# Kernel tuning notes

Hardware: AMD Instinct MI355X
Metric: run time of the kernel (lower is better)

The kernel has to match this reference:

```python
import jax, jax.numpy as jnp
import numpy as np

PI = float(np.pi)


def _layernorm(x, g, b, eps=1e-5):
    mu = jnp.mean(x, axis=-1, keepdims=True)
    var = jnp.var(x, axis=-1, keepdims=True)
    return (x - mu) * jax.lax.rsqrt(var + eps) * g + b


def setup_inputs() -> dict:
    key = jax.random.key(0)
    B, L, D, P = 4, 2048, 256, 32
    ks = jax.random.split(key, 16)

    def lin_w(k, fi, fo):
        return (jax.random.normal(k, (fi, fo), dtype=jnp.float32) / np.sqrt(fi)).astype(jnp.float32)

    inp = {
        'x': jax.random.normal(ks[0], (B, L, D), dtype=jnp.float32),
        'pos_phases': jax.random.normal(ks[1], (L, P), dtype=jnp.float32) * PI,
        'w_mem1v': lin_w(ks[2], D, P), 'b_mem1v': jnp.zeros((P,), jnp.float32),
        'w_mem1o': lin_w(ks[3], P, D), 'b_mem1o': jnp.zeros((D,), jnp.float32),
        'w_off': lin_w(ks[4], D + P, P), 'b_off': jnp.zeros((P,), jnp.float32),
        'w_key': lin_w(ks[5], D, P), 'b_key': jnp.zeros((P,), jnp.float32),
        'w_val': lin_w(ks[6], D, D), 'b_val': jnp.zeros((D,), jnp.float32),
        'w_sk1': lin_w(ks[7], 2 * D, D), 'b_sk1': jnp.zeros((D,), jnp.float32),
        'w_sk2': lin_w(ks[8], D, P), 'b_sk2': jnp.zeros((P,), jnp.float32),
        'w_gate': lin_w(ks[9], D, 1), 'b_gate': jnp.zeros((1,), jnp.float32),
        'ln_g': jnp.ones((D,), jnp.float32), 'ln_b': jnp.zeros((D,), jnp.float32),
        'w_out': lin_w(ks[10], D, D), 'b_out': jnp.zeros((D,), jnp.float32),
    }
    return inp


def reference(x, pos_phases, w_mem1v, b_mem1v, w_mem1o, b_mem1o, w_off, b_off,
              w_key, b_key, w_val, b_val, w_sk1, b_sk1, w_sk2, b_sk2,
              w_gate, b_gate, ln_g, ln_b, w_out, b_out):
    B, L, D = x.shape
    P = pos_phases.shape[-1]

    pos_cos = jnp.cos(pos_phases)  # [L,P]
    pos_sin = jnp.sin(pos_phases)

    # Memory 1: flat [B,L,P] phasor cumulative memory
    v1 = x @ w_mem1v + b_mem1v                       # [B,L,P]
    mem1_cos = jnp.cumsum(pos_cos[None] * v1, axis=1)
    mem1_sin = jnp.cumsum(pos_sin[None] * v1, axis=1)

    offset_input = jnp.concatenate([x, jnp.broadcast_to(pos_phases[None], (B, L, P))], axis=-1)
    offset = jnp.tanh(offset_input @ w_off + b_off) * PI
    oc, os = jnp.cos(offset), jnp.sin(offset)
    query_cos = pos_cos[None] * oc - pos_sin[None] * os
    query_sin = pos_sin[None] * oc + pos_cos[None] * os
    pos_ret = (mem1_cos * query_cos + mem1_sin * query_sin) / np.sqrt(P)
    pos_out = pos_ret @ w_mem1o + b_mem1o            # [B,L,D]

    # Memory 2: full [B,L,P,D] phasor KV cumulative memory
    key_phases = jnp.tanh(x @ w_key + b_key) * PI    # [B,L,P]
    key_cos, key_sin = jnp.cos(key_phases), jnp.sin(key_phases)
    values = x @ w_val + b_val                       # [B,L,D]
    store_gate = jax.nn.sigmoid(x @ w_gate + b_gate) # [B,L,1]

    positions = jnp.arange(1, L + 1, dtype=x.dtype)[None, :, None]
    context_avg = jnp.cumsum(x, axis=1) / positions
    h = jax.nn.gelu(jnp.concatenate([x, context_avg], axis=-1) @ w_sk1 + b_sk1, approximate=False)
    storage_phases = jnp.tanh(h @ w_sk2 + b_sk2) * PI  # [B,L,P]

    gated_v = values * store_gate                    # [B,L,D]
    kv_mem_cos = jnp.cumsum(jnp.cos(storage_phases)[..., None] * gated_v[:, :, None, :], axis=1)  # [B,L,P,D]
    kv_mem_sin = jnp.cumsum(jnp.sin(storage_phases)[..., None] * gated_v[:, :, None, :], axis=1)

    gate_cumsum = jnp.clip(jnp.cumsum(store_gate, axis=1), 1.0, None)  # [B,L,1]
    kv_retrieved = jnp.einsum('blpd,blp->bld', kv_mem_cos, key_cos) + \
                   jnp.einsum('blpd,blp->bld', kv_mem_sin, key_sin)
    kv_retrieved = kv_retrieved / (jnp.sqrt(gate_cumsum) * np.sqrt(P))

    combined = pos_out + kv_retrieved
    return x + _layernorm(combined, ln_g, ln_b) @ w_out + b_out
```

## Files before the change

kernel.cpp:

```cpp
#include <hip/hip_runtime.h>
#include <hip/hip_bf16.h>

constexpr int B_ = 4;
constexpr int L_ = 2048;
constexpr int D_ = 256;
constexpr int P_ = 32;
constexpr int CL = 32;
constexpr int NC = L_ / CL;

#define PI_F 3.14159265358979323846f
#define INV_SQRT_P 0.17677669529663687f

typedef __attribute__((ext_vector_type(8))) short short8_t;
typedef __attribute__((ext_vector_type(4))) float floatx4;

static __device__ inline short f2bf(float f) {
  unsigned int u;
  __builtin_memcpy(&u, &f, 4);
  unsigned int r = (u + 0x7fffu + ((u >> 16) & 1u)) >> 16;
  return (short)r;
}
static __device__ inline float bf2f(short s) {
  unsigned int u = ((unsigned int)(unsigned short)s) << 16;
  float f;
  __builtin_memcpy(&f, &u, 4);
  return f;
}

__global__ void wprep(const float* __restrict__ x, const float* __restrict__ pos,
                      const float* __restrict__ w_val, const float* __restrict__ w_mem1v,
                      const float* __restrict__ w_off, const float* __restrict__ b_off,
                      const float* __restrict__ w_key, const float* __restrict__ w_gate,
                      const float* __restrict__ w_sk1, const float* __restrict__ w_out,
                      const float* __restrict__ w_sk2, const float* __restrict__ w_mem1o,
                      short* __restrict__ WA, short* __restrict__ W1,
                      short* __restrict__ WO, short* __restrict__ W2T,
                      short* __restrict__ W1OT,
                      short* __restrict__ xbf, float* __restrict__ poff,
                      float* __restrict__ ctxsum) {
  int blk = blockIdx.x, tid = threadIdx.x;
  if (blk < 384) {
    int idx = blk * 256 + tid;
    int n = idx >> 8, k = idx & 255;
    float v;
    if (n < 256) v = w_val[k * 256 + n];
    else if (n < 288) v = w_mem1v[k * 32 + (n - 256)];
    else if (n < 320) v = w_off[k * 32 + (n - 288)];
    else if (n < 352) v = w_key[k * 32 + (n - 320)];
    else if (n == 352) v = w_gate[k];
    else v = 0.f;
    WA[idx] = f2bf(v);
  } else if (blk < 896) {
    int idx = (blk - 384) * 256 + tid;
    int n = idx >> 9, k = idx & 511;
    W1[idx] = f2bf(w_sk1[k * 256 + n]);
  } else if (blk < 1152) {
    int idx = (blk - 896) * 256 + tid;
    int n = idx >> 8, k = idx & 255;
    WO[idx] = f2bf(w_out[k * 256 + n]);
  } else if (blk < 1184) {
    int idx = (blk - 1152) * 256 + tid;
    int p = idx >> 8, k = idx & 255;
    W2T[idx] = f2bf(w_sk2[k * 32 + p]);
  } else if (blk < 1216) {
    int idx = (blk - 1184) * 256 + tid;
    int d = idx >> 5, p = idx & 31;
    W1OT[idx] = f2bf(w_mem1o[p * 256 + d]);
  } else if (blk < 3264) {
    int idx = ((blk - 1216) * 256 + tid) * 4;
    float4 v = *(const float4*)&x[idx];
    short4 o;
    o.x = f2bf(v.x); o.y = f2bf(v.y); o.z = f2bf(v.z); o.w = f2bf(v.w);
    *(short4*)&xbf[idx] = o;
  } else if (blk < 3520) {
    int idx = (blk - 3264) * 256 + tid;
    int l = idx >> 5, p = idx & 31;
    float a = b_off[p];
    for (int j = 0; j < 32; ++j) a += pos[l * 32 + j] * w_off[(256 + j) * 32 + p];
    poff[idx] = a;
  } else {
    int c2 = blk - 3520;
    int b = c2 >> 6, ch = c2 & 63;
    int xb = (b * L_ + ch * 32) * 256 + tid;
    float s = 0.f;
#pragma unroll 8
    for (int i = 0; i < 32; ++i) s += x[xb + i * 256];
    ctxsum[c2 * 256 + tid] = s;
  }
}

template <int KTILES, int NBLK, int MODE>
__global__ __launch_bounds__(256) void gemm_k(const short* __restrict__ A0,
                                              const short* __restrict__ A1,
                                              const short* __restrict__ W,
                                              const float* __restrict__ bias,
                                              const float* __restrict__ xres,
                                              float* __restrict__ outf,
                                              short* __restrict__ outb) {
  __shared__ short As[64][136];
  __shared__ short Bs[64][136];
  int tid = threadIdx.x;
  int mg = blockIdx.x / NBLK, ng = blockIdx.x % NBLK;
  int tok0 = mg * 64, n0 = ng * 64;
  int lane = tid & 63, w = tid >> 6;
  int mw = (w & 1) * 32, nw = (w >> 1) * 32;
  floatx4 acc[2][2] = {{{0.f, 0.f, 0.f, 0.f}, {0.f, 0.f, 0.f, 0.f}},
                       {{0.f, 0.f, 0.f, 0.f}, {0.f, 0.f, 0.f, 0.f}}};
  int r2 = tid >> 4, c8 = tid & 15;
  int ml = lane & 15, kq = (lane >> 4) * 8;
  const int K = KTILES * 128;

  for (int kt = 0; kt < KTILES; ++kt) {
    const short* Asrc;
    int cb;
    if (KTILES == 4) {
      Asrc = (kt < 2) ? A0 : A1;
      cb = (kt & 1) * 128;
    } else {
      Asrc = A0;
      cb = kt * 128;
    }
#pragma unroll
    for (int pass = 0; pass < 4; ++pass) {
      int row = pass * 16 + r2;
      *(short8_t*)&As[row][c8 * 8] =
          *(const short8_t*)&Asrc[(tok0 + row) * 256 + cb + c8 * 8];
      *(short8_t*)&Bs[row][c8 * 8] =
          *(const short8_t*)&W[(n0 + row) * K + kt * 128 + c8 * 8];
    }
    __syncthreads();
#pragma unroll
    for (int s = 0; s < 4; ++s) {
      short8_t a0 = *(short8_t*)&As[mw + ml][s * 32 + kq];
      short8_t a1 = *(short8_t*)&As[mw + 16 + ml][s * 32 + kq];
      short8_t b0 = *(short8_t*)&Bs[nw + ml][s * 32 + kq];
      short8_t b1 = *(short8_t*)&Bs[nw + 16 + ml][s * 32 + kq];
      acc[0][0] = __builtin_amdgcn_mfma_f32_16x16x32_bf16(a0, b0, acc[0][0], 0, 0, 0);
      acc[0][1] = __builtin_amdgcn_mfma_f32_16x16x32_bf16(a0, b1, acc[0][1], 0, 0, 0);
      acc[1][0] = __builtin_amdgcn_mfma_f32_16x16x32_bf16(a1, b0, acc[1][0], 0, 0, 0);
      acc[1][1] = __builtin_amdgcn_mfma_f32_16x16x32_bf16(a1, b1, acc[1][1], 0, 0, 0);
    }
    __syncthreads();
  }
  int col = lane & 15, rq = (lane >> 4) * 4;
#pragma unroll
  for (int nt = 0; nt < 2; ++nt) {
    int n = n0 + nw + nt * 16 + col;
    float bv = (MODE == 0) ? 0.f : bias[n];
#pragma unroll
    for (int mt = 0; mt < 2; ++mt) {
#pragma unroll
      for (int rg = 0; rg < 4; ++rg) {
        int tok = tok0 + mw + mt * 16 + rq + rg;
        float v = acc[mt][nt][rg] + bv;
        if (MODE == 0) {
          outb[tok * 384 + n] = f2bf(v);
        } else if (MODE == 1) {
          float g = 0.5f * v * (1.f + erff(v * 0.70710678118654752f));
          outb[tok * 256 + n] = f2bf(g);
        } else {
          outf[tok * 256 + n] = xres[tok * 256 + n] + v;
        }
      }
    }
  }
}

__global__ __launch_bounds__(384) void gemmA3(const short* __restrict__ xbf,
                                              const short* __restrict__ WA,
                                              const float* __restrict__ pos,
                                              const float* __restrict__ poff,
                                              const float* __restrict__ b_mem1v,
                                              const float* __restrict__ b_key,
                                              const float* __restrict__ b_gate,
                                              const float* __restrict__ b_val,
                                              float* __restrict__ m1cT,
                                              float* __restrict__ m1sT,
                                              float* __restrict__ qc,
                                              float* __restrict__ qs,
                                              short* __restrict__ K2bf,
                                              short* __restrict__ gvT,
                                              float* __restrict__ sg) {
  __shared__ float YL[32][132];
  __shared__ float gsh[32];
  int tid = threadIdx.x;
  int lane = tid & 63, w = tid >> 6;
  int ml = lane & 15, quad = lane >> 4, kq = quad * 8;
  int bc = blockIdx.x;
  int tok0 = bc * 32;
  floatx4 acc[2][4] = {};
  const short* A0p = &xbf[(tok0 + ml) * 256 + kq];
  const short* A1p = &xbf[(tok0 + 16 + ml) * 256 + kq];
  const short* Bp = &WA[(w * 64 + ml) * 256 + kq];
#pragma unroll
  for (int ks = 0; ks < 8; ++ks) {
    short8_t a0 = *(const short8_t*)(A0p + ks * 32);
    short8_t a1 = *(const short8_t*)(A1p + ks * 32);
#pragma unroll
    for (int nt = 0; nt < 4; ++nt) {
      short8_t b = *(const short8_t*)(Bp + nt * 16 * 256 + ks * 32);
      acc[0][nt] = __builtin_amdgcn_mfma_f32_16x16x32_bf16(a0, b, acc[0][nt], 0, 0, 0);
      acc[1][nt] = __builtin_amdgcn_mfma_f32_16x16x32_bf16(a1, b, acc[1][nt], 0, 0, 0);
    }
  }
  if (w >= 4) {
#pragma unroll
    for (int mt = 0; mt < 2; ++mt)
#pragma unroll
      for (int nt = 0; nt < 4; ++nt) {
        int col = (w - 4) * 64 + nt * 16 + ml;
#pragma unroll
        for (int r = 0; r < 4; ++r)
          YL[mt * 16 + quad * 4 + r][col] = acc[mt][nt][r];
      }
  }
  __syncthreads();
  if (tid < 256) {
#pragma unroll
    for (int it = 0; it < 4; ++it) {
      int idx = it * 256 + tid;
      int t = idx >> 5, p = idx & 31;
      int tok = tok0 + t, l = tok & (L_ - 1);
      int b = tok >> 11;
      float v1 = YL[t][p] + b_mem1v[p];
      float ph = pos[l * 32 + p];
      float pc = cosf(ph), ps = sinf(ph);
      int idxT = (b * 32 + p) * L_ + l;
      m1cT[idxT] = pc * v1;
      m1sT[idxT] = ps * v1;
      float off = tanhf(YL[t][32 + p] + poff[l * 32 + p]) * PI_F;
      float oc = cosf(off), os = sinf(off);
      int gidx = tok * 32 + p;
      qc[gidx] = pc * oc - ps * os;
      qs[gidx] = ps * oc + pc * os;
      float kp = tanhf(YL[t][64 + p] + b_key[p]) * PI_F;
      K2bf[tok * 64 + p] = f2bf(cosf(kp));
      K2bf[tok * 64 + 32 + p] = f2bf(sinf(kp));
      if (p == 0) {
        float g = 1.f / (1.f + expf(-(YL[t][96] + b_gate[0])));
        sg[tok] = g;
        gsh[t] = g;
      }
    }
  }
  __syncthreads();
  if (w < 4) {
#pragma unroll
    for (int nt = 0; nt < 4; ++nt) {
      int d = w * 64 + nt * 16 + ml;
      float bv = b_val[d];
#pragma unroll
      for (int mt = 0; mt < 2; ++mt) {
        int t0 = mt * 16 + quad * 4;
        short4 o;
        o.x = f2bf((acc[mt][nt][0] + bv) * gsh[t0 + 0]);
        o.y = f2bf((acc[mt][nt][1] + bv) * gsh[t0 + 1]);
        o.z = f2bf((acc[mt][nt][2] + bv) * gsh[t0 + 2]);
        o.w = f2bf((acc[mt][nt][3] + bv) * gsh[t0 + 3]);
        *(short4*)&gvT[(bc * 256 + d) * 32 + t0] = o;
      }
    }
  }
}

__global__ void scan_all(float* __restrict__ m1cT, float* __restrict__ m1sT,
                         float* __restrict__ sg, const float* __restrict__ x,
                         const float* __restrict__ ctxsum, short* __restrict__ ctxbf) {
  int blk = blockIdx.x;
  int tid = threadIdx.x;
  if (blk >= 260) {
    int c2 = blk - 260;
    int b = c2 >> 6, ch = c2 & 63;
    float run = 0.f;
    int sb = b * 64 * 256 + tid;
    for (int c = 0; c < ch; ++c) run += ctxsum[sb + c * 256];
    int xb = (b * L_ + ch * 32) * 256 + tid;
#pragma unroll 8
    for (int i = 0; i < 32; ++i) {
      run += x[xb + i * 256];
      int l = ch * 32 + i;
      ctxbf[xb + i * 256] = f2bf(run / (float)(l + 1));
    }
    return;
  }
  int lane = tid & 63, wid = tid >> 6;
  __shared__ float wsum[4];
  float carry = 0.f;
  float* arr;
  int base;
  if (blk < 256) {
    arr = (blk < 128) ? m1cT : m1sT;
    base = (blk & 127) * L_;
  } else {
    arr = sg;
    base = (blk - 256) * L_;
  }
  float v[8];
#pragma unroll
  for (int i = 0; i < 8; ++i) v[i] = arr[base + i * 256 + tid];
#pragma unroll
  for (int i = 0; i < 8; ++i) {
    float vv = v[i];
#pragma unroll
    for (int off = 1; off < 64; off <<= 1) {
      float n = __shfl_up(vv, off, 64);
      if (lane >= off) vv += n;
    }
    if (lane == 63) wsum[wid] = vv;
    __syncthreads();
    float add = carry;
    for (int w = 0; w < wid; ++w) add += wsum[w];
    arr[base + i * 256 + tid] = vv + add;
    carry += wsum[0] + wsum[1] + wsum[2] + wsum[3];
    __syncthreads();
  }
}

__global__ __launch_bounds__(256) void kernelCD(const short* __restrict__ hs,
                                                const short* __restrict__ W2T,
                                                const float* __restrict__ b_sk2,
                                                const short* __restrict__ gvT,
                                                short* __restrict__ SPbf,
                                                short* __restrict__ UT) {
  __shared__ __align__(16) short SPL[64][40];
  int tid = threadIdx.x;
  int bc = blockIdx.x;
  int tok0 = bc * 32;
  int lane = tid & 63, w = tid >> 6;
  int ml = lane & 15, quad = lane >> 4, kq = quad * 8;
  int th = w & 1, ph = w >> 1;
  floatx4 pacc = {};
#pragma unroll
  for (int s = 0; s < 8; ++s) {
    short8_t a = *(const short8_t*)&hs[(tok0 + th * 16 + ml) * 256 + s * 32 + kq];
    short8_t b0 = *(const short8_t*)&W2T[(ph * 16 + ml) * 256 + s * 32 + kq];
    pacc = __builtin_amdgcn_mfma_f32_16x16x32_bf16(a, b0, pacc, 0, 0, 0);
  }
  {
    int p = ph * 16 + ml;
    float bs = b_sk2[p];
#pragma unroll
    for (int r = 0; r < 4; ++r) {
      int tl = th * 16 + quad * 4 + r;
      int tok = tok0 + tl;
      float sp = tanhf(pacc[r] + bs) * PI_F;
      short c = f2bf(cosf(sp)), s = f2bf(sinf(sp));
      SPL[p][tl] = c;
      SPL[32 + p][tl] = s;
      SPbf[tok * 64 + p] = c;
      SPbf[tok * 64 + 32 + p] = s;
    }
  }
  __syncthreads();
  short8_t a[4];
#pragma unroll
  for (int mt = 0; mt < 4; ++mt) a[mt] = *(short8_t*)&SPL[mt * 16 + ml][kq];
  floatx4 acc[4][4] = {};
#pragma unroll
  for (int nt = 0; nt < 4; ++nt) {
    short8_t b = *(const short8_t*)&gvT[(bc * 256 + w * 64 + nt * 16 + ml) * 32 + kq];
#pragma unroll
    for (int mt = 0; mt < 4; ++mt)
      acc[mt][nt] = __builtin_amdgcn_mfma_f32_16x16x32_bf16(a[mt], b, acc[mt][nt], 0, 0, 0);
  }
#pragma unroll
  for (int mt = 0; mt < 4; ++mt)
#pragma unroll
    for (int nt = 0; nt < 4; ++nt)
#pragma unroll
      for (int r = 0; r < 4; ++r) {
        int q = mt * 16 + quad * 4 + r;
        int d = w * 64 + nt * 16 + ml;
        UT[(bc * 256 + d) * 64 + q] = f2bf(acc[mt][nt][r]);
      }
}

__global__ void kernelE(short* __restrict__ UT) {
  int tid = blockIdx.x * 256 + threadIdx.x;
  int q = tid & 63;
  int d = (tid >> 6) & 255;
  int b = tid >> 14;
  int base = ((b * NC) * 256 + d) * 64 + q;
  const int cs = 256 * 64;
  short v[64];
#pragma unroll
  for (int c = 0; c < 64; ++c) v[c] = UT[base + c * cs];
  float run = 0.f;
#pragma unroll
  for (int c = 0; c < 64; ++c) {
    UT[base + c * cs] = f2bf(run);
    run += bf2f(v[c]);
  }
}

__global__ __launch_bounds__(512) void kernelFG(const short* __restrict__ UT,
                                                const short* __restrict__ SPbf,
                                                const short* __restrict__ K2bf,
                                                const short* __restrict__ gvT,
                                                const float* __restrict__ sgc,
                                                const float* __restrict__ m1cT,
                                                const float* __restrict__ m1sT,
                                                const float* __restrict__ qc,
                                                const float* __restrict__ qs,
                                                const short* __restrict__ W1OT,
                                                const float* __restrict__ b_mem1o,
                                                const float* __restrict__ ln_g,
                                                const float* __restrict__ ln_b,
                                                short* __restrict__ cbn) {
  __shared__ __align__(16) short SL[32][40];
  __shared__ __align__(16) short PR[32][40];
  __shared__ float CMB[32][260];
  __shared__ float scl[32], mu_s[32], rs_s[32];
  int tid = threadIdx.x;
  int bc = blockIdx.x;
  int lbase = bc * CL;
  int bb = bc >> 6, lloc = (bc & 63) * 32;
  if (tid < 32) scl[tid] = rsqrtf(fmaxf(sgc[lbase + tid], 1.f)) * INV_SQRT_P;
#pragma unroll
  for (int it = 0; it < 2; ++it) {
    int i = it * 512 + tid;
    int p = i >> 5, t = i & 31;
    int gT = (bb * 32 + p) * L_ + lloc + t;
    int g = (lbase + t) * 32 + p;
    PR[t][p] = f2bf((m1cT[gT] * qc[g] + m1sT[gT] * qs[g]) * INV_SQRT_P);
  }
  int lane = tid & 63, w = tid >> 6;
  int ml = lane & 15, quad = lane >> 4, kq = quad * 8;
  int d0 = w * 32;
  floatx4 acc[2][2] = {};
  short8_t ka0 = *(const short8_t*)&K2bf[(lbase + ml) * 64 + kq];
  short8_t ka1 = *(const short8_t*)&K2bf[(lbase + 16 + ml) * 64 + kq];
  short8_t kb0 = *(const short8_t*)&K2bf[(lbase + ml) * 64 + 32 + kq];
  short8_t kb1 = *(const short8_t*)&K2bf[(lbase + 16 + ml) * 64 + 32 + kq];
#pragma unroll
  for (int nt = 0; nt < 2; ++nt) {
    short8_t b = *(const short8_t*)&UT[(bc * 256 + d0 + nt * 16 + ml) * 64 + kq];
    acc[0][nt] = __builtin_amdgcn_mfma_f32_16x16x32_bf16(ka0, b, acc[0][nt], 0, 0, 0);
    acc[1][nt] = __builtin_amdgcn_mfma_f32_16x16x32_bf16(ka1, b, acc[1][nt], 0, 0, 0);
  }
  if (w == 0) {
    floatx4 sacc[2][2] = {};
#pragma unroll
    for (int ks2 = 0; ks2 < 2; ++ks2) {
      short8_t a0 = (ks2 == 0) ? ka0 : kb0;
      short8_t a1 = (ks2 == 0) ? ka1 : kb1;
      short8_t b0 = *(const short8_t*)&SPbf[(lbase + ml) * 64 + ks2 * 32 + kq];
      short8_t b1 = *(const short8_t*)&SPbf[(lbase + 16 + ml) * 64 + ks2 * 32 + kq];
      sacc[0][0] = __builtin_amdgcn_mfma_f32_16x16x32_bf16(a0, b0, sacc[0][0], 0, 0, 0);
      sacc[0][1] = __builtin_amdgcn_mfma_f32_16x16x32_bf16(a0, b1, sacc[0][1], 0, 0, 0);
      sacc[1][0] = __builtin_amdgcn_mfma_f32_16x16x32_bf16(a1, b0, sacc[1][0], 0, 0, 0);
      sacc[1][1] = __builtin_amdgcn_mfma_f32_16x16x32_bf16(a1, b1, sacc[1][1], 0, 0, 0);
    }
#pragma unroll
    for (int mt = 0; mt < 2; ++mt)
#pragma unroll
      for (int nt = 0; nt < 2; ++nt)
#pragma unroll
        for (int r = 0; r < 4; ++r) {
          int trow = mt * 16 + quad * 4 + r;
          int scol = nt * 16 + ml;
          float v = (scol <= trow) ? sacc[mt][nt][r] : 0.f;
          SL[trow][scol] = f2bf(v);
        }
  }
  __syncthreads();
#pragma unroll
  for (int nt = 0; nt < 2; ++nt) {
    short8_t b = *(const short8_t*)&UT[(bc * 256 + d0 + nt * 16 + ml) * 64 + 32 + kq];
    acc[0][nt] = __builtin_amdgcn_mfma_f32_16x16x32_bf16(kb0, b, acc[0][nt], 0, 0, 0);
    acc[1][nt] = __builtin_amdgcn_mfma_f32_16x16x32_bf16(kb1, b, acc[1][nt], 0, 0, 0);
  }
  {
    short8_t a0 = *(short8_t*)&SL[ml][kq];
    short8_t a1 = *(short8_t*)&SL[16 + ml][kq];
#pragma unroll
    for (int nt = 0; nt < 2; ++nt) {
      short8_t b = *(const short8_t*)&gvT[(bc * 256 + d0 + nt * 16 + ml) * 32 + kq];
      acc[0][nt] = __builtin_amdgcn_mfma_f32_16x16x32_bf16(a0, b, acc[0][nt], 0, 0, 0);
      acc[1][nt] = __builtin_amdgcn_mfma_f32_16x16x32_bf16(a1, b, acc[1][nt], 0, 0, 0);
    }
  }
  floatx4 macc[2][2] = {};
  {
    short8_t a0 = *(short8_t*)&PR[ml][kq];
    short8_t a1 = *(short8_t*)&PR[16 + ml][kq];
#pragma unroll
    for (int nt = 0; nt < 2; ++nt) {
      short8_t b = *(const short8_t*)&W1OT[(d0 + nt * 16 + ml) * 32 + kq];
      macc[0][nt] = __builtin_amdgcn_mfma_f32_16x16x32_bf16(a0, b, macc[0][nt], 0, 0, 0);
      macc[1][nt] = __builtin_amdgcn_mfma_f32_16x16x32_bf16(a1, b, macc[1][nt], 0, 0, 0);
    }
  }
#pragma unroll
  for (int mt = 0; mt < 2; ++mt)
#pragma unroll
    for (int nt = 0; nt < 2; ++nt) {
      int d = d0 + nt * 16 + ml;
      float bm = b_mem1o[d];
#pragma unroll
      for (int r = 0; r < 4; ++r) {
        int t = mt * 16 + quad * 4 + r;
        CMB[t][d] = acc[mt][nt][r] * scl[t] + macc[mt][nt][r] + bm;
      }
    }
  __syncthreads();
  {
    int t = tid >> 4, g = tid & 15;
    float s = 0.f, s2 = 0.f;
#pragma unroll
    for (int j = 0; j < 16; ++j) {
      float v = CMB[t][g + j * 16];
      s += v;
      s2 += v * v;
    }
#pragma unroll
    for (int m = 1; m < 16; m <<= 1) {
      s += __shfl_xor(s, m, 64);
      s2 += __shfl_xor(s2, m, 64);
    }
    if (g == 0) {
      float mu = s / (float)D_;
      float var = s2 / (float)D_ - mu * mu;
      mu_s[t] = mu;
      rs_s[t] = rsqrtf(var + 1e-5f);
    }
  }
  __syncthreads();
  {
    int d = tid & 255, th = tid >> 8;
    float lg = ln_g[d], lb = ln_b[d];
#pragma unroll
    for (int i = 0; i < 16; ++i) {
      int t = th * 16 + i;
      cbn[(lbase + t) * 256 + d] = f2bf((CMB[t][d] - mu_s[t]) * rs_s[t] * lg + lb);
    }
  }
}

extern "C" void kernel_launch(void* const* d_in, const int* in_sizes, int n_in,
                              void* d_out, int out_size, void* d_ws, size_t ws_size,
                              hipStream_t stream) {
  const float* x = (const float*)d_in[0];
  const float* pos = (const float*)d_in[1];
  const float* w_mem1v = (const float*)d_in[2];
  const float* b_mem1v = (const float*)d_in[3];
  const float* w_mem1o = (const float*)d_in[4];
  const float* b_mem1o = (const float*)d_in[5];
  const float* w_off = (const float*)d_in[6];
  const float* b_off = (const float*)d_in[7];
  const float* w_key = (const float*)d_in[8];
  const float* b_key = (const float*)d_in[9];
  const float* w_val = (const float*)d_in[10];
  const float* b_val = (const float*)d_in[11];
  const float* w_sk1 = (const float*)d_in[12];
  const float* b_sk1 = (const float*)d_in[13];
  const float* w_sk2 = (const float*)d_in[14];
  const float* b_sk2 = (const float*)d_in[15];
  const float* w_gate = (const float*)d_in[16];
  const float* b_gate = (const float*)d_in[17];
  const float* ln_g = (const float*)d_in[18];
  const float* ln_b = (const float*)d_in[19];
  const float* w_out = (const float*)d_in[20];
  const float* b_out = (const float*)d_in[21];
  float* out = (float*)d_out;
  float* ws = (float*)d_ws;

  const int BLP = B_ * L_ * P_;
  const int BLD = B_ * L_ * D_;
  float* m1cT = ws;
  float* m1sT = m1cT + BLP;
  float* qc = m1sT + BLP;
  float* qs = qc + BLP;
  float* sg = qs + BLP;
  float* poff = sg + B_ * L_;
  float* ctxsum = poff + L_ * P_;
  short* UT = (short*)(ctxsum + B_ * 64 * 256);
  short* xbf = UT + (size_t)B_ * NC * 256 * 64;
  short* cbn = xbf;
  short* ctxbf = xbf + BLD;
  short* hs = ctxbf + BLD;
  short* gvT = hs + BLD;
  short* K2bf = gvT + BLD;
  short* SPbf = K2bf + B_ * L_ * 64;
  short* WA = SPbf + B_ * L_ * 64;
  short* W1 = WA + 384 * 256;
  short* WO = W1 + 256 * 512;
  short* W2T = WO + 256 * 256;
  short* W1OT = W2T + 32 * 256;

  wprep<<<3776, 256, 0, stream>>>(x, pos, w_val, w_mem1v, w_off, b_off, w_key, w_gate,
                                  w_sk1, w_out, w_sk2, w_mem1o, WA, W1, WO, W2T, W1OT,
                                  xbf, poff, ctxsum);
  gemmA3<<<256, 384, 0, stream>>>(xbf, WA, pos, poff, b_mem1v, b_key, b_gate, b_val,
                                  m1cT, m1sT, qc, qs, K2bf, gvT, sg);
  scan_all<<<516, 256, 0, stream>>>(m1cT, m1sT, sg, x, ctxsum, ctxbf);
  gemm_k<4, 4, 1><<<128 * 4, 256, 0, stream>>>(xbf, ctxbf, W1, b_sk1, nullptr, nullptr, hs);
  kernelCD<<<(B_ * L_) / 32, 256, 0, stream>>>(hs, W2T, b_sk2, gvT, SPbf, UT);
  kernelE<<<256, 256, 0, stream>>>(UT);
  kernelFG<<<B_ * NC, 512, 0, stream>>>(UT, SPbf, K2bf, gvT, sg, m1cT, m1sT, qc, qs,
                                        W1OT, b_mem1o, ln_g, ln_b, cbn);
  gemm_k<2, 4, 2><<<128 * 4, 256, 0, stream>>>(cbn, nullptr, WO, b_out, x, out, nullptr);
}
```

Baseline: 180.3 us.

## Halve tile sizes across GEMM and chunk kernels to double grid parallelism

The generic GEMM is replaced by a 32-token tile variant, launched on twice as many blocks. gemmA3 now processes 16 tokens per block, and kernelCD splits the D dimension across two blocks, with only one of them writing SPbf. UT stores are vectorised to short4, the ctxsum prefix loop is unrolled by eight, and occupancy hints are added to launch_bounds. The aim is to fill more of the MI355X's compute units on these small launches, at the cost of more redundant weight loads and lower MFMA reuse per block.

```diff
diff --git a/kernel.cpp b/kernel.cpp
--- a/kernel.cpp
+++ b/kernel.cpp
@@ -76,6 +76,7 @@
     int idx = (blk - 3264) * 256 + tid;
     int l = idx >> 5, p = idx & 31;
     float a = b_off[p];
+#pragma unroll 8
     for (int j = 0; j < 32; ++j) a += pos[l * 32 + j] * w_off[(256 + j) * 32 + p];
     poff[idx] = a;
   } else {
@@ -89,25 +90,24 @@
   }
 }
 
-template <int KTILES, int NBLK, int MODE>
-__global__ __launch_bounds__(256) void gemm_k(const short* __restrict__ A0,
-                                              const short* __restrict__ A1,
-                                              const short* __restrict__ W,
-                                              const float* __restrict__ bias,
-                                              const float* __restrict__ xres,
-                                              float* __restrict__ outf,
-                                              short* __restrict__ outb) {
-  __shared__ short As[64][136];
+template <int KTILES, int MODE>
+__global__ __launch_bounds__(256, 4) void gemm32(const short* __restrict__ A0,
+                                                 const short* __restrict__ A1,
+                                                 const short* __restrict__ W,
+                                                 const float* __restrict__ bias,
+                                                 const float* __restrict__ xres,
+                                                 float* __restrict__ outf,
+                                                 short* __restrict__ outb) {
+  __shared__ short As[32][136];
   __shared__ short Bs[64][136];
   int tid = threadIdx.x;
-  int mg = blockIdx.x / NBLK, ng = blockIdx.x % NBLK;
-  int tok0 = mg * 64, n0 = ng * 64;
+  int mg = blockIdx.x >> 2, ng = blockIdx.x & 3;
+  int tok0 = mg * 32, n0 = ng * 64;
   int lane = tid & 63, w = tid >> 6;
-  int mw = (w & 1) * 32, nw = (w >> 1) * 32;
-  floatx4 acc[2][2] = {{{0.f, 0.f, 0.f, 0.f}, {0.f, 0.f, 0.f, 0.f}},
-                       {{0.f, 0.f, 0.f, 0.f}, {0.f, 0.f, 0.f, 0.f}}};
+  int nw = w * 16;
+  floatx4 acc[2] = {{0.f, 0.f, 0.f, 0.f}, {0.f, 0.f, 0.f, 0.f}};
   int r2 = tid >> 4, c8 = tid & 15;
-  int ml = lane & 15, kq = (lane >> 4) * 8;
+  int ml = lane & 15, quad = lane >> 4, kq = quad * 8;
   const int K = KTILES * 128;
 
   for (int kt = 0; kt < KTILES; ++kt) {
@@ -121,103 +121,94 @@
       cb = kt * 128;
     }
 #pragma unroll
-    for (int pass = 0; pass < 4; ++pass) {
+    for (int pass = 0; pass < 2; ++pass) {
       int row = pass * 16 + r2;
       *(short8_t*)&As[row][c8 * 8] =
           *(const short8_t*)&Asrc[(tok0 + row) * 256 + cb + c8 * 8];
+    }
+#pragma unroll
+    for (int pass = 0; pass < 4; ++pass) {
+      int row = pass * 16 + r2;
       *(short8_t*)&Bs[row][c8 * 8] =
           *(const short8_t*)&W[(n0 + row) * K + kt * 128 + c8 * 8];
     }
     __syncthreads();
 #pragma unroll
     for (int s = 0; s < 4; ++s) {
-      short8_t a0 = *(short8_t*)&As[mw + ml][s * 32 + kq];
-      short8_t a1 = *(short8_t*)&As[mw + 16 + ml][s * 32 + kq];
+      short8_t a0 = *(short8_t*)&As[ml][s * 32 + kq];
+      short8_t a1 = *(short8_t*)&As[16 + ml][s * 32 + kq];
       short8_t b0 = *(short8_t*)&Bs[nw + ml][s * 32 + kq];
-      short8_t b1 = *(short8_t*)&Bs[nw + 16 + ml][s * 32 + kq];
-      acc[0][0] = __builtin_amdgcn_mfma_f32_16x16x32_bf16(a0, b0, acc[0][0], 0, 0, 0);
-      acc[0][1] = __builtin_amdgcn_mfma_f32_16x16x32_bf16(a0, b1, acc[0][1], 0, 0, 0);
-      acc[1][0] = __builtin_amdgcn_mfma_f32_16x16x32_bf16(a1, b0, acc[1][0], 0, 0, 0);
-      acc[1][1] = __builtin_amdgcn_mfma_f32_16x16x32_bf16(a1, b1, acc[1][1], 0, 0, 0);
+      acc[0] = __builtin_amdgcn_mfma_f32_16x16x32_bf16(a0, b0, acc[0], 0, 0, 0);
+      acc[1] = __builtin_amdgcn_mfma_f32_16x16x32_bf16(a1, b0, acc[1], 0, 0, 0);
     }
     __syncthreads();
   }
-  int col = lane & 15, rq = (lane >> 4) * 4;
-#pragma unroll
-  for (int nt = 0; nt < 2; ++nt) {
-    int n = n0 + nw + nt * 16 + col;
-    float bv = (MODE == 0) ? 0.f : bias[n];
-#pragma unroll
-    for (int mt = 0; mt < 2; ++mt) {
-#pragma unroll
-      for (int rg = 0; rg < 4; ++rg) {
-        int tok = tok0 + mw + mt * 16 + rq + rg;
-        float v = acc[mt][nt][rg] + bv;
-        if (MODE == 0) {
-          outb[tok * 384 + n] = f2bf(v);
-        } else if (MODE == 1) {
-          float g = 0.5f * v * (1.f + erff(v * 0.70710678118654752f));
-          outb[tok * 256 + n] = f2bf(g);
-        } else {
-          outf[tok * 256 + n] = xres[tok * 256 + n] + v;
-        }
+  int n = n0 + nw + ml;
+  float bv = bias ? bias[n] : 0.f;
+#pragma unroll
+  for (int mt = 0; mt < 2; ++mt) {
+#pragma unroll
+    for (int rg = 0; rg < 4; ++rg) {
+      int tok = tok0 + mt * 16 + quad * 4 + rg;
+      float v = acc[mt][rg] + bv;
+      if (MODE == 1) {
+        float g = 0.5f * v * (1.f + erff(v * 0.70710678118654752f));
+        outb[tok * 256 + n] = f2bf(g);
+      } else {
+        outf[tok * 256 + n] = xres[tok * 256 + n] + v;
       }
     }
   }
 }
 
-__global__ __launch_bounds__(384) void gemmA3(const short* __restrict__ xbf,
-                                              const short* __restrict__ WA,
-                                              const float* __restrict__ pos,
-                                              const float* __restrict__ poff,
-                                              const float* __restrict__ b_mem1v,
-                                              const float* __restrict__ b_key,
-                                              const float* __restrict__ b_gate,
-                                              const float* __restrict__ b_val,
-                                              float* __restrict__ m1cT,
-                                              float* __restrict__ m1sT,
-                                              float* __restrict__ qc,
-                                              float* __restrict__ qs,
-                                              short* __restrict__ K2bf,
-                                              short* __restrict__ gvT,
-                                              float* __restrict__ sg) {
-  __shared__ float YL[32][132];
-  __shared__ float gsh[32];
+__global__ __launch_bounds__(384, 3) void gemmA3(const short* __restrict__ xbf,
+                                                 const short* __restrict__ WA,
+                                                 const float* __restrict__ pos,
+                                                 const float* __restrict__ poff,
+                                                 const float* __restrict__ b_mem1v,
+                                                 const float* __restrict__ b_key,
+                                                 const float* __restrict__ b_gate,
+                                                 const float* __restrict__ b_val,
+                                                 float* __restrict__ m1cT,
+                                                 float* __restrict__ m1sT,
+                                                 float* __restrict__ qc,
+                                                 float* __restrict__ qs,
+                                                 short* __restrict__ K2bf,
+                                                 short* __restrict__ gvT,
+                                                 float* __restrict__ sg) {
+  __shared__ float YL[16][132];
+  __shared__ float gsh[16];
   int tid = threadIdx.x;
   int lane = tid & 63, w = tid >> 6;
   int ml = lane & 15, quad = lane >> 4, kq = quad * 8;
   int bc = blockIdx.x;
-  int tok0 = bc * 32;
-  floatx4 acc[2][4] = {};
+  int bc32 = bc >> 1, half = bc & 1;
+  int tok0 = bc * 16;
+  floatx4 acc[4] = {};
   const short* A0p = &xbf[(tok0 + ml) * 256 + kq];
-  const short* A1p = &xbf[(tok0 + 16 + ml) * 256 + kq];
   const short* Bp = &WA[(w * 64 + ml) * 256 + kq];
 #pragma unroll
   for (int ks = 0; ks < 8; ++ks) {
     short8_t a0 = *(const short8_t*)(A0p + ks * 32);
-    short8_t a1 = *(const short8_t*)(A1p + ks * 32);
 #pragma unroll
     for (int nt = 0; nt < 4; ++nt) {
       short8_t b = *(const short8_t*)(Bp + nt * 16 * 256 + ks * 32);
-      acc[0][nt] = __builtin_amdgcn_mfma_f32_16x16x32_bf16(a0, b, acc[0][nt], 0, 0, 0);
-      acc[1][nt] = __builtin_amdgcn_mfma_f32_16x16x32_bf16(a1, b, acc[1][nt], 0, 0, 0);
+      acc[nt] = __builtin_amdgcn_mfma_f32_16x16x32_bf16(a0, b, acc[nt], 0, 0, 0);
     }
   }
   if (w >= 4) {
 #pragma unroll
-    for (int mt = 0; mt < 2; ++mt)
-#pragma unroll
-      for (int nt = 0; nt < 4; ++nt) {
-        int col = (w - 4) * 64 + nt * 16 + ml;
-#pragma unroll
-        for (int r = 0; r < 4; ++r)
-          YL[mt * 16 + quad * 4 + r][col] = acc[mt][nt][r];
-      }
+    for (int nt = 0; nt < 4; ++nt) {
+      int col = (w - 4) * 64 + nt * 16 + ml;
+#pragma unroll
+      for (int r = 0; r < 4; ++r)
+        YL[quad * 4 + r][col] = acc[nt][r];
+    }
   }
   __syncthreads();
   if (tid < 256) {
 #pragma unroll
-    for (int it = 0; it < 4; ++it) {
+    for (int it = 0; it < 2; ++it) {
       int idx = it * 256 + tid;
       int t = idx >> 5, p = idx & 31;
       int tok = tok0 + t, l = tok & (L_ - 1);
@@ -249,16 +240,13 @@
     for (int nt = 0; nt < 4; ++nt) {
       int d = w * 64 + nt * 16 + ml;
       float bv = b_val[d];
-#pragma unroll
-      for (int mt = 0; mt < 2; ++mt) {
-        int t0 = mt * 16 + quad * 4;
-        short4 o;
-        o.x = f2bf((acc[mt][nt][0] + bv) * gsh[t0 + 0]);
-        o.y = f2bf((acc[mt][nt][1] + bv) * gsh[t0 + 1]);
-        o.z = f2bf((acc[mt][nt][2] + bv) * gsh[t0 + 2]);
-        o.w = f2bf((acc[mt][nt][3] + bv) * gsh[t0 + 3]);
-        *(short4*)&gvT[(bc * 256 + d) * 32 + t0] = o;
-      }
+      int t0 = quad * 4;
+      short4 o;
+      o.x = f2bf((acc[nt][0] + bv) * gsh[t0 + 0]);
+      o.y = f2bf((acc[nt][1] + bv) * gsh[t0 + 1]);
+      o.z = f2bf((acc[nt][2] + bv) * gsh[t0 + 2]);
+      o.w = f2bf((acc[nt][3] + bv) * gsh[t0 + 3]);
+      *(short4*)&gvT[(bc32 * 256 + d) * 32 + half * 16 + t0] = o;
     }
   }
 }
@@ -273,7 +261,19 @@
     int b = c2 >> 6, ch = c2 & 63;
     float run = 0.f;
     int sb = b * 64 * 256 + tid;
-    for (int c = 0; c < ch; ++c) run += ctxsum[sb + c * 256];
+    int c = 0;
+    for (; c + 8 <= ch; c += 8) {
+      float t0 = ctxsum[sb + (c + 0) * 256];
+      float t1 = ctxsum[sb + (c + 1) * 256];
+      float t2 = ctxsum[sb + (c + 2) * 256];
+      float t3 = ctxsum[sb + (c + 3) * 256];
+      float t4 = ctxsum[sb + (c + 4) * 256];
+      float t5 = ctxsum[sb + (c + 5) * 256];
+      float t6 = ctxsum[sb + (c + 6) * 256];
+      float t7 = ctxsum[sb + (c + 7) * 256];
+      run += ((t0 + t1) + (t2 + t3)) + ((t4 + t5) + (t6 + t7));
+    }
+    for (; c < ch; ++c) run += ctxsum[sb + c * 256];
     int xb = (b * L_ + ch * 32) * 256 + tid;
 #pragma unroll 8
     for (int i = 0; i < 32; ++i) {
@@ -316,15 +316,15 @@
   }
 }
 
-__global__ __launch_bounds__(256) void kernelCD(const short* __restrict__ hs,
-                                                const short* __restrict__ W2T,
-                                                const float* __restrict__ b_sk2,
-                                                const short* __restrict__ gvT,
-                                                short* __restrict__ SPbf,
-                                                short* __restrict__ UT) {
+__global__ __launch_bounds__(256, 2) void kernelCD(const short* __restrict__ hs,
+                                                   const short* __restrict__ W2T,
+                                                   const float* __restrict__ b_sk2,
+                                                   const short* __restrict__ gvT,
+                                                   short* __restrict__ SPbf,
+                                                   short* __restrict__ UT) {
   __shared__ __align__(16) short SPL[64][40];
   int tid = threadIdx.x;
-  int bc = blockIdx.x;
+  int bc = blockIdx.x >> 1, dh = blockIdx.x & 1;
   int tok0 = bc * 32;
   int lane = tid & 63, w = tid >> 6;
   int ml = lane & 15, quad = lane >> 4, kq = quad * 8;
@@ -347,18 +347,21 @@
       short c = f2bf(cosf(sp)), s = f2bf(sinf(sp));
       SPL[p][tl] = c;
       SPL[32 + p][tl] = s;
-      SPbf[tok * 64 + p] = c;
-      SPbf[tok * 64 + 32 + p] = s;
+      if (dh == 0) {
+        SPbf[tok * 64 + p] = c;
+        SPbf[tok * 64 + 32 + p] = s;
+      }
     }
   }
   __syncthreads();
   short8_t a[4];
 #pragma unroll
   for (int mt = 0; mt < 4; ++mt) a[mt] = *(short8_t*)&SPL[mt * 16 + ml][kq];
-  floatx4 acc[4][4] = {};
-#pragma unroll
-  for (int nt = 0; nt < 4; ++nt) {
-    short8_t b = *(const short8_t*)&gvT[(bc * 256 + w * 64 + nt * 16 + ml) * 32 + kq];
+  floatx4 acc[4][2] = {};
+#pragma unroll
+  for (int nt = 0; nt < 2; ++nt) {
+    int d = dh * 128 + w * 32 + nt * 16 + ml;
+    short8_t b = *(const short8_t*)&gvT[(bc * 256 + d) * 32 + kq];
 #pragma unroll
     for (int mt = 0; mt < 4; ++mt)
       acc[mt][nt] = __builtin_amdgcn_mfma_f32_16x16x32_bf16(a[mt], b, acc[mt][nt], 0, 0, 0);
@@ -366,13 +369,15 @@
 #pragma unroll
   for (int mt = 0; mt < 4; ++mt)
 #pragma unroll
-    for (int nt = 0; nt < 4; ++nt)
-#pragma unroll
-      for (int r = 0; r < 4; ++r) {
-        int q = mt * 16 + quad * 4 + r;
-        int d = w * 64 + nt * 16 + ml;
-        UT[(bc * 256 + d) * 64 + q] = f2bf(acc[mt][nt][r]);
-      }
+    for (int nt = 0; nt < 2; ++nt) {
+      int d = dh * 128 + w * 32 + nt * 16 + ml;
+      short4 o;
+      o.x = f2bf(acc[mt][nt][0]);
+      o.y = f2bf(acc[mt][nt][1]);
+      o.z = f2bf(acc[mt][nt][2]);
+      o.w = f2bf(acc[mt][nt][3]);
+      *(short4*)&UT[(bc * 256 + d) * 64 + mt * 16 + quad * 4] = o;
+    }
 }
 
 __global__ void kernelE(short* __restrict__ UT) {
@@ -393,20 +398,20 @@
   }
 }
 
-__global__ __launch_bounds__(512) void kernelFG(const short* __restrict__ UT,
-                                                const short* __restrict__ SPbf,
-                                                const short* __restrict__ K2bf,
-                                                const short* __restrict__ gvT,
-                                                const float* __restrict__ sgc,
-                                                const float* __restrict__ m1cT,
-                                                const float* __restrict__ m1sT,
-                                                const float* __restrict__ qc,
-                                                const float* __restrict__ qs,
-                                                const short* __restrict__ W1OT,
-                                                const float* __restrict__ b_mem1o,
-                                                const float* __restrict__ ln_g,
-                                                const float* __restrict__ ln_b,
-                                                short* __restrict__ cbn) {
+__global__ __launch_bounds__(512, 2) void kernelFG(const short* __restrict__ UT,
+                                                   const short* __restrict__ SPbf,
+                                                   const short* __restrict__ K2bf,
+                                                   const short* __restrict__ gvT,
+                                                   const float* __restrict__ sgc,
+                                                   const float* __restrict__ m1cT,
+                                                   const float* __restrict__ m1sT,
+                                                   const float* __restrict__ qc,
+                                                   const float* __restrict__ qs,
+                                                   const short* __restrict__ W1OT,
+                                                   const float* __restrict__ b_mem1o,
+                                                   const float* __restrict__ ln_g,
+                                                   const float* __restrict__ ln_b,
+                                                   short* __restrict__ cbn) {
   __shared__ __align__(16) short SL[32][40];
   __shared__ __align__(16) short PR[32][40];
   __shared__ float CMB[32][260];
@@ -591,13 +596,13 @@
   wprep<<<3776, 256, 0, stream>>>(x, pos, w_val, w_mem1v, w_off, b_off, w_key, w_gate,
                                   w_sk1, w_out, w_sk2, w_mem1o, WA, W1, WO, W2T, W1OT,
                                   xbf, poff, ctxsum);
-  gemmA3<<<256, 384, 0, stream>>>(xbf, WA, pos, poff, b_mem1v, b_key, b_gate, b_val,
+  gemmA3<<<512, 384, 0, stream>>>(xbf, WA, pos, poff, b_mem1v, b_key, b_gate, b_val,
                                   m1cT, m1sT, qc, qs, K2bf, gvT, sg);
   scan_all<<<516, 256, 0, stream>>>(m1cT, m1sT, sg, x, ctxsum, ctxbf);
-  gemm_k<4, 4, 1><<<128 * 4, 256, 0, stream>>>(xbf, ctxbf, W1, b_sk1, nullptr, nullptr, hs);
-  kernelCD<<<(B_ * L_) / 32, 256, 0, stream>>>(hs, W2T, b_sk2, gvT, SPbf, UT);
+  gemm32<4, 1><<<256 * 4, 256, 0, stream>>>(xbf, ctxbf, W1, b_sk1, nullptr, nullptr, hs);
+  kernelCD<<<512, 256, 0, stream>>>(hs, W2T, b_sk2, gvT, SPbf, UT);
   kernelE<<<256, 256, 0, stream>>>(UT);
   kernelFG<<<B_ * NC, 512, 0, stream>>>(UT, SPbf, K2bf, gvT, sg, m1cT, m1sT, qc, qs,
                                         W1OT, b_mem1o, ln_g, ln_b, cbn);
-  gemm_k<2, 4, 2><<<128 * 4, 256, 0, stream>>>(cbn, nullptr, WO, b_out, x, out, nullptr);
-}
+  gemm32<2, 2><<<256 * 4, 256, 0, stream>>>(cbn, nullptr, WO, b_out, x, out, nullptr);
+}
```

New measurement: 171.5 us. 4.9% less time.
